# Kernel optimization log

Hardware: AMD Instinct MI355X
Metric: run time of the kernel (lower is better)

## Reference

```python
import jax, jax.numpy as jnp
import numpy as np

ACT_BIT = 8
W_BIT = 8
EPS = 1e-8


def ste_round(x):
    # straight-through round (matches torch STE quant autograd)
    return x + jax.lax.stop_gradient(jnp.round(x) - x)


def quant_act(x):
    """Per-tensor symmetric 8-bit activation quantization (HAWQ QuantAct)."""
    n = 2 ** (ACT_BIT - 1) - 1  # 127
    x_max = jax.lax.stop_gradient(jnp.max(jnp.abs(x)))
    scale = jnp.maximum(x_max, EPS) / n
    x_int = jnp.clip(ste_round(x / scale), -n - 1, n)
    return x_int * scale, scale


def quant_linear(x_q, act_scale, weight, bias):
    """Per-channel symmetric 8-bit weight quant + integer matmul + fused dequant."""
    n = 2 ** (W_BIT - 1) - 1  # 127
    w_max = jax.lax.stop_gradient(jnp.max(jnp.abs(weight), axis=1, keepdims=True))  # [out,1]
    w_scale = jnp.maximum(w_max, EPS) / n                                            # [out,1]
    w_int = jnp.clip(ste_round(weight / w_scale), -n - 1, n)                         # [out,in]
    bias_scale = w_scale[:, 0] * act_scale                                           # [out]
    b_int = ste_round(bias / bias_scale)                                             # [out]
    x_int = x_q / act_scale                                   # integer-valued float, [..., in]
    out_int = jnp.einsum('...i,oi->...o', x_int, w_int)       # int8-domain GEMM in float
    return (out_int + b_int) * bias_scale                     # fused dequant


def setup_inputs() -> dict:
    key = jax.random.key(0)
    k1, k2, k3 = jax.random.split(key, 3)
    L, B, Q, D, O = 6, 8, 1024, 1024, 1024
    hs = jax.random.normal(k1, (L, B, Q, D), dtype=jnp.float32)
    weight = jax.random.normal(k2, (O, D), dtype=jnp.float32) * 0.02
    bias = jax.random.normal(k3, (O,), dtype=jnp.float32) * 0.02
    return {"hs": hs, "weight": weight, "bias": bias}


def reference(hs, weight, bias):
    x_q, act_scale = quant_act(hs)
    return quant_linear(x_q, act_scale, weight, bias)
```

## Files before the change

kernel.cpp:

```cpp
#include <hip/hip_runtime.h>
#include <stdint.h>

typedef int i32x4 __attribute__((ext_vector_type(4)));
typedef int i32x16 __attribute__((ext_vector_type(16)));

#define K_DIM 1024
#define BM 256
#define BN 256
#define BKK 64
#define NKT (K_DIM / BKK)


__device__ __forceinline__ int quant1(float v, float inv) {
  float t = rintf(v * inv);
  t = fminf(fmaxf(t, -128.0f), 127.0f);
  return (int)t;
}

__device__ __forceinline__ void gld_lds16(const signed char* g, signed char* l) {
  typedef const __attribute__((address_space(1))) unsigned int* gp_t;
  typedef __attribute__((address_space(3))) unsigned int* lp_t;
  __builtin_amdgcn_global_load_lds((gp_t)(const void*)g, (lp_t)(void*)l, 16, 0, 0);
}

#define SB __builtin_amdgcn_sched_barrier(0)
#define BAR __builtin_amdgcn_s_barrier()

__global__ void absmax_part(const float* __restrict__ x, float* __restrict__ parts,
                            long long n4) {
  long long i = (long long)blockIdx.x * blockDim.x + threadIdx.x;
  const long long stride = (long long)gridDim.x * blockDim.x;
  const float4* x4 = (const float4*)x;
  float m = 0.0f;
  for (; i < n4; i += stride) {
    float4 v = x4[i];
    m = fmaxf(m, fmaxf(fmaxf(fabsf(v.x), fabsf(v.y)), fmaxf(fabsf(v.z), fabsf(v.w))));
  }
#pragma unroll
  for (int off = 32; off > 0; off >>= 1) m = fmaxf(m, __shfl_down(m, off, 64));
  __shared__ float sm[4];
  const int lane = threadIdx.x & 63, wid = threadIdx.x >> 6;
  if (lane == 0) sm[wid] = m;
  __syncthreads();
  if (threadIdx.x == 0)
    parts[blockIdx.x] = fmaxf(fmaxf(sm[0], sm[1]), fmaxf(sm[2], sm[3]));
}

__global__ void absmax_fin(const float* __restrict__ parts, unsigned int* __restrict__ amax_u,
                           int nparts) {
  const int t = threadIdx.x;
  float m = 0.0f;
  for (int i = t; i < nparts; i += 256) m = fmaxf(m, parts[i]);
#pragma unroll
  for (int off = 32; off > 0; off >>= 1) m = fmaxf(m, __shfl_down(m, off, 64));
  __shared__ float sm[4];
  const int lane = t & 63, wid = t >> 6;
  if (lane == 0) sm[wid] = m;
  __syncthreads();
  if (t == 0)
    amax_u[0] = __float_as_uint(fmaxf(fmaxf(sm[0], sm[1]), fmaxf(sm[2], sm[3])));
}

__global__ void wquant_kernel(const float* __restrict__ w, const float* __restrict__ bias,
                              const unsigned int* __restrict__ amax_u,
                              signed char* __restrict__ wq,
                              float* __restrict__ bscale, float* __restrict__ bint) {
  const int o = blockIdx.x;
  const int t = threadIdx.x;
  float4 v = ((const float4*)(w + (size_t)o * K_DIM))[t];
  float m = fmaxf(fmaxf(fabsf(v.x), fabsf(v.y)), fmaxf(fabsf(v.z), fabsf(v.w)));
#pragma unroll
  for (int off = 32; off > 0; off >>= 1) m = fmaxf(m, __shfl_down(m, off, 64));
  __shared__ float sm[4];
  __shared__ float s_scale;
  const int lane = t & 63, wid = t >> 6;
  if (lane == 0) sm[wid] = m;
  __syncthreads();
  if (t == 0) {
    float wm = fmaxf(fmaxf(sm[0], sm[1]), fmaxf(sm[2], sm[3]));
    float wsc = fmaxf(wm, 1e-8f) / 127.0f;
    float asc = fmaxf(__uint_as_float(*amax_u), 1e-8f) / 127.0f;
    float bsc = wsc * asc;
    bscale[o] = bsc;
    bint[o] = rintf(bias[o] / bsc);
    s_scale = wsc;
  }
  __syncthreads();
  const float inv = 1.0f / s_scale;
  int q0 = quant1(v.x, inv), q1 = quant1(v.y, inv), q2 = quant1(v.z, inv), q3 = quant1(v.w, inv);
  unsigned int p = (unsigned)(q0 & 255) | ((unsigned)(q1 & 255) << 8) |
                   ((unsigned)(q2 & 255) << 16) | ((unsigned)(q3 & 255) << 24);
  const int F = o >> 5, T = t >> 3;
  const int l = (o & 31) | (((t >> 2) & 1) << 5);
  const int j = (t << 2) & 15;
  *(unsigned int*)(wq + (((size_t)(F * 32 + T)) << 10) + (l << 4) + j) = p;
}

__global__ __launch_bounds__(256) void aquant_kernel(
    const float* __restrict__ x, const unsigned int* __restrict__ amax_u,
    uint4* __restrict__ q16) {
  __shared__ unsigned int limg[4096];
  const float asc = fmaxf(__uint_as_float(*amax_u), 1e-8f) / 127.0f;
  const float inv = 1.0f / asc;
  const int b = blockIdx.x;
  const int F32 = b >> 1, bh = b & 1;
  const int t = threadIdx.x;
  const int r = t >> 4, kq = t & 15;
  const float* rowp = x + (((size_t)b * 16 + r) << 10);
#pragma unroll
  for (int rep = 0; rep < 16; ++rep) {
    const int fi = rep * 16 + kq;
    float4 v = ((const float4*)rowp)[fi];
    int q0 = quant1(v.x, inv), q1 = quant1(v.y, inv), q2 = quant1(v.z, inv), q3 = quant1(v.w, inv);
    unsigned int p = (unsigned)(q0 & 255) | ((unsigned)(q1 & 255) << 8) |
                     ((unsigned)(q2 & 255) << 16) | ((unsigned)(q3 & 255) << 24);
    const int k0 = fi << 2;
    const int T32 = k0 >> 5;
    const int hi = (k0 >> 4) & 1;
    const int j = k0 & 15;
    limg[(((T32 << 1) | hi) << 6) + (r << 2) + (j >> 2)] = p;
  }
  __syncthreads();
  const uint4* src = (const uint4*)limg;
#pragma unroll
  for (int rep2 = 0; rep2 < 4; ++rep2) {
    const int e = rep2 * 256 + t;
    const int T32 = e >> 5, hs = (e >> 4) & 1, rr = e & 15;
    q16[(((size_t)(F32 * 32 + T32)) << 6) + (hs * 32 + bh * 16 + rr)] = src[e];
  }
}

__global__ __launch_bounds__(512, 2) void gemm_kernel(
    const signed char* __restrict__ A, const signed char* __restrict__ W,
    const float* __restrict__ bscale, const float* __restrict__ bint,
    float* __restrict__ out, int M, int N, int K) {
  extern __shared__ __align__(16) signed char smem[];
  signed char* Abase = smem;

  const int nwg = gridDim.x;
  const int orig = blockIdx.x;
  const int wgid = (orig & 7) * (nwg >> 3) + (orig >> 3);
  const int nbn = N / BN;
  const int bm = wgid / nbn;
  const int bn = wgid % nbn;
  const int m0 = bm * BM, n0 = bn * BN;

  const int tid = threadIdx.x;
  const int lane = tid & 63;
  const int wid = tid >> 6;
  const int wr = wid >> 2;
  const int wc = wid & 3;

  const signed char* gaf =
      A + (((size_t)((m0 >> 5) + (wid >> 1)) * 32 + (wid & 1)) << 10) + (lane << 4);
  const size_t fs8 = (size_t)128 << 10;
  const signed char* gbf =
      W + (((size_t)((n0 >> 5) + wc * 2) * 32) << 10) + (lane << 4);

  i32x16 acc[4][2];
#pragma unroll
  for (int i = 0; i < 4; i++)
#pragma unroll
    for (int j = 0; j < 2; j++)
#pragma unroll
      for (int r = 0; r < 16; r++) acc[i][j][r] = 0;

  i32x4 af[4][2];
  i32x4 bA[2][2], bB[2][2];

#define LOADB(L, tt)                                                           \
  do {                                                                         \
    L[0][0] = *(const i32x4*)(gbf + (((size_t)(tt) * 2 + 0) << 10));           \
    L[0][1] = *(const i32x4*)(gbf + (((size_t)(tt) * 2 + 1) << 10));           \
    L[1][0] = *(const i32x4*)(gbf + ((size_t)1 << 15) + (((size_t)(tt) * 2 + 0) << 10)); \
    L[1][1] = *(const i32x4*)(gbf + ((size_t)1 << 15) + (((size_t)(tt) * 2 + 1) << 10)); \
  } while (0)

#define ISSUEA(tt)                                                             \
  do {                                                                         \
    gld_lds16(gaf + ((size_t)(tt) << 11),                                      \
              Abase + ((((tt) & 3) * 16 + wid) << 10));                        \
    gld_lds16(gaf + fs8 + ((size_t)(tt) << 11),                                \
              Abase + ((((tt) & 3) * 16 + wid + 8) << 10));                    \
  } while (0)

#define RD_A(t)                                                                \
  do {                                                                         \
    _Pragma("unroll") for (int m_ = 0; m_ < 4; m_++)                           \
      _Pragma("unroll") for (int k_ = 0; k_ < 2; k_++)                         \
        af[m_][k_] = *(const i32x4*)(Abase + ((((t) & 3) * 16 +                \
                        (wr * 4 + m_) * 2 + k_) << 10) + (lane << 4));         \
  } while (0)

#define MFMA16(U)                                                              \
  do {                                                                         \
    __builtin_amdgcn_s_setprio(1);                                             \
    _Pragma("unroll") for (int m_ = 0; m_ < 4; m_++)                           \
      _Pragma("unroll") for (int g_ = 0; g_ < 2; g_++)                         \
        _Pragma("unroll") for (int k_ = 0; k_ < 2; k_++)                       \
          acc[m_][g_] = __builtin_amdgcn_mfma_i32_32x32x32_i8(                 \
              af[m_][k_], U[g_][k_], acc[m_][g_], 0, 0, 0);                    \
    __builtin_amdgcn_s_setprio(0);                                             \
  } while (0)

#define TILE(t, U, L, DOB, DOA, VMW, DOVM)                                     \
  do {                                                                         \
    if (DOB) LOADB(L, (t) + 1);                                                \
    if (DOA) ISSUEA((t) + 3);                                                  \
    SB;                                                                        \
    RD_A(t);                                                                   \
    MFMA16(U);                                                                 \
    if (DOVM) { asm volatile("s_waitcnt " VMW ::: "memory"); }                 \
    SB; BAR; SB;                                                               \
  } while (0)

  ISSUEA(0); ISSUEA(1); ISSUEA(2);
  LOADB(bA, 0);
  asm volatile("s_waitcnt vmcnt(8)" ::: "memory");
  SB; BAR; SB;

  TILE(0,  bA, bB, 1, 1, "vmcnt(8)", 1);
  TILE(1,  bB, bA, 1, 1, "vmcnt(8)", 1);
  TILE(2,  bA, bB, 1, 1, "vmcnt(8)", 1);
  TILE(3,  bB, bA, 1, 1, "vmcnt(8)", 1);
  TILE(4,  bA, bB, 1, 1, "vmcnt(8)", 1);
  TILE(5,  bB, bA, 1, 1, "vmcnt(8)", 1);
  TILE(6,  bA, bB, 1, 1, "vmcnt(8)", 1);
  TILE(7,  bB, bA, 1, 1, "vmcnt(8)", 1);
  TILE(8,  bA, bB, 1, 1, "vmcnt(8)", 1);
  TILE(9,  bB, bA, 1, 1, "vmcnt(8)", 1);
  TILE(10, bA, bB, 1, 1, "vmcnt(8)", 1);
  TILE(11, bB, bA, 1, 1, "vmcnt(8)", 1);
  TILE(12, bA, bB, 1, 1, "vmcnt(8)", 1);
  TILE(13, bB, bA, 1, 0, "vmcnt(6)", 1);
  TILE(14, bA, bB, 1, 0, "vmcnt(4)", 1);
  TILE(15, bB, bA, 0, 0, "", 0);

#undef TILE
#undef MFMA16
#undef RD_A
#undef ISSUEA
#undef LOADB

  const int cl = lane & 31;
  const int hi4 = (lane >> 5) << 2;
#pragma unroll
  for (int g = 0; g < 2; g++) {
    const int col = n0 + (wc * 2 + g) * 32 + cl;
    const float bs = bscale[col];
    const float bi = bint[col];
#pragma unroll
    for (int m = 0; m < 4; m++) {
      const int rowb = m0 + (wr * 4 + m) * 32 + hi4;
#pragma unroll
      for (int r = 0; r < 16; r++) {
        const int row = rowb + (r & 3) + ((r >> 2) << 3);
        out[(size_t)row * N + col] = ((float)acc[m][g][r] + bi) * bs;
      }
    }
  }
}

extern "C" void kernel_launch(void* const* d_in, const int* in_sizes, int n_in,
                              void* d_out, int out_size, void* d_ws, size_t ws_size,
                              hipStream_t stream) {
  const float* hs = (const float*)d_in[0];
  const float* w = (const float*)d_in[1];
  const float* bias = (const float*)d_in[2];
  float* out = (float*)d_out;

  const long long n = (long long)in_sizes[0];
  const int K = K_DIM;
  const int O = in_sizes[2];
  const int M = (int)(n / K);

  char* ws = (char*)d_ws;
  unsigned int* amax_u = (unsigned int*)ws;
  float* parts = (float*)(ws + 1024);
  float* bscale = (float*)(ws + 16384);
  float* bint = (float*)(ws + 20480);
  signed char* wq = (signed char*)(ws + 65536);
  signed char* xq = (signed char*)(ws + 65536 + 1048576);

  hipFuncSetAttribute((const void*)gemm_kernel,
                      hipFuncAttributeMaxDynamicSharedMemorySize, 65536);

  const long long n4 = n / 4;
  absmax_part<<<2048, 256, 0, stream>>>(hs, parts, n4);
  absmax_fin<<<1, 256, 0, stream>>>(parts, amax_u, 2048);
  wquant_kernel<<<O, 256, 0, stream>>>(w, bias, amax_u, wq, bscale, bint);
  aquant_kernel<<<M / 16, 256, 0, stream>>>(hs, amax_u, (uint4*)xq);

  const int nblocks = (M / BM) * (O / BN);
  gemm_kernel<<<nblocks, 512, 65536, stream>>>(xq, wq, bscale, bint, out, M, O, K);
}
```

Before: 187.1 us.

## Make GEMM persistent with three tiles per block and cross-tile A prefetch

The GEMM launch shrinks from 768 blocks to 256, and each block processes three M-tiles spaced 2048 rows apart in sequence. The A-tile prefetch ring carries over between jobs, so the next job's first tiles load during the current job's tail and epilogue, and the pipeline ramp only happens once. Grid size and M stride are hardcoded to this shape (M=49152, N=1024), which drops generality and may leave some CUs idle if 256 blocks map unevenly.

Measured after the change: 242.5 us. +29.6%, slower.

```diff
diff --git a/kernel.cpp b/kernel.cpp
--- a/kernel.cpp
+++ b/kernel.cpp
@@ -7,8 +7,8 @@
 #define K_DIM 1024
 #define BM 256
 #define BN 256
-#define BKK 64
-#define NKT (K_DIM / BKK)
+#define NKT 16
+#define NJOB 3
 
 
 __device__ __forceinline__ int quant1(float v, float inv) {
@@ -137,13 +137,11 @@
   extern __shared__ __align__(16) signed char smem[];
   signed char* Abase = smem;
 
-  const int nwg = gridDim.x;
   const int orig = blockIdx.x;
-  const int wgid = (orig & 7) * (nwg >> 3) + (orig >> 3);
-  const int nbn = N / BN;
-  const int bm = wgid / nbn;
-  const int bn = wgid % nbn;
-  const int m0 = bm * BM, n0 = bn * BN;
+  const int wg = (orig & 7) * 96 + (orig >> 3);
+  const int bn = wg & 3;
+  const int bm0 = wg >> 2;
+  const int m0 = bm0 * BM, n0 = bn * BN;
 
   const int tid = threadIdx.x;
   const int lane = tid & 63;
@@ -176,12 +174,13 @@
     L[1][1] = *(const i32x4*)(gbf + ((size_t)1 << 15) + (((size_t)(tt) * 2 + 1) << 10)); \
   } while (0)
 
-#define ISSUEA(tt)                                                             \
-  do {                                                                         \
-    gld_lds16(gaf + ((size_t)(tt) << 11),                                      \
-              Abase + ((((tt) & 3) * 16 + wid) << 10));                        \
-    gld_lds16(gaf + fs8 + ((size_t)(tt) << 11),                                \
-              Abase + ((((tt) & 3) * 16 + wid + 8) << 10));                    \
+#define ISSUEA_J(jj, tl)                                                       \
+  do {                                                                         \
+    const size_t jo_ = (size_t)(jj) << 21;                    \
+    gld_lds16(gaf + jo_ + ((size_t)(tl) << 11),                                \
+              Abase + ((((tl) & 3) * 16 + wid) << 10));                        \
+    gld_lds16(gaf + jo_ + fs8 + ((size_t)(tl) << 11),                          \
+              Abase + ((((tl) & 3) * 16 + wid + 8) << 10));                    \
   } while (0)
 
 #define RD_A(t)                                                                \
@@ -203,62 +202,106 @@
     __builtin_amdgcn_s_setprio(0);                                             \
   } while (0)
 
-#define TILE(t, U, L, DOB, DOA, VMW, DOVM)                                     \
-  do {                                                                         \
-    if (DOB) LOADB(L, (t) + 1);                                                \
-    if (DOA) ISSUEA((t) + 3);                                                  \
+#define TILEF(lt, U, L, JJ, TL)                                                \
+  do {                                                                         \
+    LOADB(L, ((lt) + 1) & 15);                                                 \
+    ISSUEA_J(JJ, TL);                                                          \
     SB;                                                                        \
-    RD_A(t);                                                                   \
+    RD_A(lt);                                                                  \
+    MFMA16(U);                                                                 \
+    asm volatile("s_waitcnt vmcnt(8)" ::: "memory");                           \
+    SB; BAR; SB;                                                               \
+  } while (0)
+
+#define TILET(lt, U, L, DOB, VMW, DOVM)                                        \
+  do {                                                                         \
+    if (DOB) LOADB(L, (lt) + 1);                                               \
+    SB;                                                                        \
+    RD_A(lt);                                                                  \
     MFMA16(U);                                                                 \
     if (DOVM) { asm volatile("s_waitcnt " VMW ::: "memory"); }                 \
     SB; BAR; SB;                                                               \
   } while (0)
 
-  ISSUEA(0); ISSUEA(1); ISSUEA(2);
+#define EPIL(jj)                                                               \
+  do {                                                                         \
+    const int m0j_ = m0 + (jj) * 2048;                                         \
+    const int cl_ = lane & 31;                                                 \
+    const int hi4_ = (lane >> 5) << 2;                                         \
+    _Pragma("unroll") for (int g = 0; g < 2; g++) {                            \
+      const int col = n0 + (wc * 2 + g) * 32 + cl_;                            \
+      const float bs = bscale[col];                                            \
+      const float bi = bint[col];                                              \
+      _Pragma("unroll") for (int m = 0; m < 4; m++) {                          \
+        const int rowb = m0j_ + (wr * 4 + m) * 32 + hi4_;                      \
+        _Pragma("unroll") for (int r = 0; r < 16; r++) {                       \
+          const int row = rowb + (r & 3) + ((r >> 2) << 3);                    \
+          out[(size_t)row * N + col] = ((float)acc[m][g][r] + bi) * bs;        \
+        }                                                                      \
+      }                                                                        \
+    }                                                                          \
+  } while (0)
+
+#define ZEROACC                                                                \
+  do {                                                                         \
+    _Pragma("unroll") for (int i = 0; i < 4; i++)                              \
+      _Pragma("unroll") for (int j2 = 0; j2 < 2; j2++)                         \
+        _Pragma("unroll") for (int r = 0; r < 16; r++) acc[i][j2][r] = 0;      \
+  } while (0)
+
+  ISSUEA_J(0, 0); ISSUEA_J(0, 1); ISSUEA_J(0, 2);
   LOADB(bA, 0);
   asm volatile("s_waitcnt vmcnt(8)" ::: "memory");
   SB; BAR; SB;
 
-  TILE(0,  bA, bB, 1, 1, "vmcnt(8)", 1);
-  TILE(1,  bB, bA, 1, 1, "vmcnt(8)", 1);
-  TILE(2,  bA, bB, 1, 1, "vmcnt(8)", 1);
-  TILE(3,  bB, bA, 1, 1, "vmcnt(8)", 1);
-  TILE(4,  bA, bB, 1, 1, "vmcnt(8)", 1);
-  TILE(5,  bB, bA, 1, 1, "vmcnt(8)", 1);
-  TILE(6,  bA, bB, 1, 1, "vmcnt(8)", 1);
-  TILE(7,  bB, bA, 1, 1, "vmcnt(8)", 1);
-  TILE(8,  bA, bB, 1, 1, "vmcnt(8)", 1);
-  TILE(9,  bB, bA, 1, 1, "vmcnt(8)", 1);
-  TILE(10, bA, bB, 1, 1, "vmcnt(8)", 1);
-  TILE(11, bB, bA, 1, 1, "vmcnt(8)", 1);
-  TILE(12, bA, bB, 1, 1, "vmcnt(8)", 1);
-  TILE(13, bB, bA, 1, 0, "vmcnt(6)", 1);
-  TILE(14, bA, bB, 1, 0, "vmcnt(4)", 1);
-  TILE(15, bB, bA, 0, 0, "", 0);
-
-#undef TILE
+#pragma unroll 1
+  for (int j = 0; j < 2; ++j) {
+    TILEF(0,  bA, bB, j, 3);
+    TILEF(1,  bB, bA, j, 4);
+    TILEF(2,  bA, bB, j, 5);
+    TILEF(3,  bB, bA, j, 6);
+    TILEF(4,  bA, bB, j, 7);
+    TILEF(5,  bB, bA, j, 8);
+    TILEF(6,  bA, bB, j, 9);
+    TILEF(7,  bB, bA, j, 10);
+    TILEF(8,  bA, bB, j, 11);
+    TILEF(9,  bB, bA, j, 12);
+    TILEF(10, bA, bB, j, 13);
+    TILEF(11, bB, bA, j, 14);
+    TILEF(12, bA, bB, j, 15);
+    TILEF(13, bB, bA, j + 1, 0);
+    TILEF(14, bA, bB, j + 1, 1);
+    TILEF(15, bB, bA, j + 1, 2);
+    EPIL(j);
+    ZEROACC;
+  }
+
+  TILEF(0,  bA, bB, 2, 3);
+  TILEF(1,  bB, bA, 2, 4);
+  TILEF(2,  bA, bB, 2, 5);
+  TILEF(3,  bB, bA, 2, 6);
+  TILEF(4,  bA, bB, 2, 7);
+  TILEF(5,  bB, bA, 2, 8);
+  TILEF(6,  bA, bB, 2, 9);
+  TILEF(7,  bB, bA, 2, 10);
+  TILEF(8,  bA, bB, 2, 11);
+  TILEF(9,  bB, bA, 2, 12);
+  TILEF(10, bA, bB, 2, 13);
+  TILEF(11, bB, bA, 2, 14);
+  TILEF(12, bA, bB, 2, 15);
+  TILET(13, bB, bA, 1, "vmcnt(6)", 1);
+  TILET(14, bA, bB, 1, "vmcnt(4)", 1);
+  TILET(15, bB, bA, 0, "", 0);
+  EPIL(2);
+
+#undef ZEROACC
+#undef EPIL
+#undef TILET
+#undef TILEF
 #undef MFMA16
 #undef RD_A
-#undef ISSUEA
+#undef ISSUEA_J
 #undef LOADB
-
-  const int cl = lane & 31;
-  const int hi4 = (lane >> 5) << 2;
-#pragma unroll
-  for (int g = 0; g < 2; g++) {
-    const int col = n0 + (wc * 2 + g) * 32 + cl;
-    const float bs = bscale[col];
-    const float bi = bint[col];
-#pragma unroll
-    for (int m = 0; m < 4; m++) {
-      const int rowb = m0 + (wr * 4 + m) * 32 + hi4;
-#pragma unroll
-      for (int r = 0; r < 16; r++) {
-        const int row = rowb + (r & 3) + ((r >> 2) << 3);
-        out[(size_t)row * N + col] = ((float)acc[m][g][r] + bi) * bs;
-      }
-    }
-  }
 }
 
 extern "C" void kernel_launch(void* const* d_in, const int* in_sizes, int n_in,
@@ -291,6 +334,5 @@
   wquant_kernel<<<O, 256, 0, stream>>>(w, bias, amax_u, wq, bscale, bint);
   aquant_kernel<<<M / 16, 256, 0, stream>>>(hs, amax_u, (uint4*)xq);
 
-  const int nblocks = (M / BM) * (O / BN);
-  gemm_kernel<<<nblocks, 512, 65536, stream>>>(xq, wq, bscale, bint, out, M, O, K);
-}
+  gemm_kernel<<<256, 512, 65536, stream>>>(xq, wq, bscale, bint, out, M, O, K);
+}
```
